# Kernel tuning notes

Hardware: AMD Instinct MI355X
Metric: run time of the kernel (lower is better)

## Reference

```python
import jax, jax.numpy as jnp
import numpy as np

DIM = 128
IND_DIM = 5
HEADS = 4
DIM_HEAD = 32
HIDDEN = HEADS * DIM_HEAD  # 128
SCALE = DIM_HEAD ** -0.5


def setup_inputs() -> dict:
    key = jax.random.key(0)
    ks = jax.random.split(key, 6)
    b, n = 1, 512
    x = jax.random.normal(ks[0], (b, DIM, n), dtype=jnp.float32)
    indicator = jax.random.normal(ks[1], (b, IND_DIM, n, n), dtype=jnp.float32)
    # conv1d kernels with kernel_size=1 are just (out, in) matrices
    w_qkv = jax.random.normal(ks[2], (HIDDEN * 3, DIM), dtype=jnp.float32) * (DIM ** -0.5)
    w_ind = jax.random.normal(ks[3], (HIDDEN * 2, IND_DIM), dtype=jnp.float32) * (IND_DIM ** -0.5)
    w_out = jax.random.normal(ks[4], (DIM, HIDDEN), dtype=jnp.float32) * (HIDDEN ** -0.5)
    b_out = jax.random.normal(ks[5], (DIM,), dtype=jnp.float32) * 0.01
    return {"x": x, "indicator": indicator, "w_qkv": w_qkv,
            "w_ind": w_ind, "w_out": w_out, "b_out": b_out}


def reference(x, indicator, w_qkv, w_ind, w_out, b_out):
    b, c, n = x.shape
    h, dh = HEADS, DIM_HEAD
    # pointwise conv = channel matmul
    qkv = jnp.einsum('oc,bcn->bon', w_qkv, x)  # (b, 3*hidden, n)
    q, k, v = jnp.split(qkv, 3, axis=1)
    q = q.reshape(b, h, dh, n)
    k = k.reshape(b, h, dh, n)
    v = v.reshape(b, h, dh, n)
    ind = jnp.einsum('oc,bcij->boij', w_ind, indicator)  # (b, 2*hidden, n, n)
    ind_q, ind_k = jnp.split(ind, 2, axis=1)
    ind_q = ind_q.reshape(b, h, dh, n, n)
    ind_k = ind_k.reshape(b, h, dh, n, n)
    qq = (q[..., :, None] + ind_q) * SCALE        # (b, h, dh, n, n)
    kk = k[..., None, :] + ind_k                   # (b, h, dh, n, n)
    sim = jnp.einsum('bhdij,bhdij->bhij', qq, kk)  # (b, h, n, n)
    attn = jax.nn.softmax(sim, axis=-1)
    out = jnp.einsum('bhij,bhdj->bhdi', attn, v)   # (b, h, dh, n)
    out = out.reshape(b, h * dh, n)
    return jnp.einsum('oc,bcn->bon', w_out, out) + b_out[None, :, None]
```

## Files before the change

kernel.cpp:

```cpp
#include <hip/hip_runtime.h>
#include <math.h>

#define N      512
#define DIMC   128
#define HEADS  4
#define DH     32
#define INDC   5
#define SCALE  0.1767766952966369f

#define QKV_ROWS 384
#define AQ_BASE  384
#define AK_BASE  404
#define TOT_ROWS 424
#define NROW_BLK (TOT_ROWS / 4)

#define ROWS_F   0
#define MHS_F    (TOT_ROWS * N)
#define WOUTT_F  (MHS_F + 64)

__global__ __launch_bounds__(256) void pre_kernel(const float* __restrict__ w_qkv,
                                                  const float* __restrict__ w_ind,
                                                  const float* __restrict__ x,
                                                  const float* __restrict__ w_out,
                                                  float* __restrict__ ws) {
    const int bx = blockIdx.x;
    const int t  = threadIdx.x;
    float* rows   = ws + ROWS_F;
    float* MhS    = ws + MHS_F;
    float* w_outT = ws + WOUTT_F;

    if (bx == NROW_BLK) {
        __shared__ float mraw[HEADS * INDC * INDC];
        if (t < HEADS * INDC * INDC) {
            const int h = t / 25, c = (t / 5) % 5, cc = t % 5;
            float acc = 0.f;
            for (int d = 0; d < DH; ++d)
                acc = fmaf(w_ind[(h * DH + d) * INDC + c],
                           w_ind[(DIMC + h * DH + d) * INDC + cc], acc);
            mraw[t] = acc;
        }
        __syncthreads();
        if (t < 64) {
            const int h = t >> 4, idx = t & 15;
            const int PC[10]  = {0, 0, 0, 0, 1, 1, 1, 2, 2, 3};
            const int PCC[10] = {1, 2, 3, 4, 2, 3, 4, 3, 4, 4};
            float s = 0.f;
            if (idx < 5) {
                s = mraw[h * 25 + idx * 5 + idx];
            } else if (idx < 15) {
                const int c = PC[idx - 5], cc = PCC[idx - 5];
                s = mraw[h * 25 + c * 5 + cc] + mraw[h * 25 + cc * 5 + c];
            }
            MhS[h * 16 + idx] = s;
        }
        for (int idx = t; idx < DIMC * DIMC; idx += 256) {
            const int o = idx >> 7, c = idx & 127;
            w_outT[c * DIMC + o] = w_out[idx];
        }
        return;
    }

    __shared__ float ws2[4 * DIMC];
    const int o0 = bx * 4;
    for (int idx = t; idx < 4 * DIMC; idx += 256) {
        const int r = idx & 3, m = idx >> 2;
        const int row = o0 + r;
        float val;
        if (row < QKV_ROWS) {
            val = w_qkv[row * DIMC + m];
        } else if (row < AK_BASE) {
            const int rr = row - AQ_BASE, h = rr / INDC, c = rr % INDC;
            float acc = 0.f;
            for (int d = 0; d < DH; ++d)
                acc = fmaf(w_qkv[(h * DH + d) * DIMC + m],
                           w_ind[(DIMC + h * DH + d) * INDC + c], acc);
            val = acc;
        } else {
            const int rr = row - AK_BASE, h = rr / INDC, c = rr % INDC;
            float acc = 0.f;
            for (int d = 0; d < DH; ++d)
                acc = fmaf(w_qkv[(DIMC + h * DH + d) * DIMC + m],
                           w_ind[(h * DH + d) * INDC + c], acc);
            val = acc;
        }
        ws2[m * 4 + r] = val;
    }
    __syncthreads();

    const float2* x2 = (const float2*)x;
    float2 acc[4] = {{0.f,0.f},{0.f,0.f},{0.f,0.f},{0.f,0.f}};
#pragma unroll 8
    for (int c = 0; c < DIMC; ++c) {
        const float2 xv = x2[c * 256 + t];
        const float4 wv = *(const float4*)(ws2 + c * 4);
        acc[0].x = fmaf(wv.x, xv.x, acc[0].x); acc[0].y = fmaf(wv.x, xv.y, acc[0].y);
        acc[1].x = fmaf(wv.y, xv.x, acc[1].x); acc[1].y = fmaf(wv.y, xv.y, acc[1].y);
        acc[2].x = fmaf(wv.z, xv.x, acc[2].x); acc[2].y = fmaf(wv.z, xv.y, acc[2].y);
        acc[3].x = fmaf(wv.w, xv.x, acc[3].x); acc[3].y = fmaf(wv.w, xv.y, acc[3].y);
    }
#pragma unroll
    for (int r = 0; r < 4; ++r)
        ((float2*)(rows + (o0 + r) * N))[t] = acc[r];
}

__global__ __launch_bounds__(256) void attn_kernel(const float* __restrict__ ws,
                                                   const float* __restrict__ ind,
                                                   const float* __restrict__ b_out,
                                                   float* __restrict__ out) {
    const int i    = blockIdx.x;
    const int t    = threadIdx.x;
    const int lane = t & 63;
    const int wave = t >> 6;

    const float* rows   = ws + ROWS_F;
    const float* MhS    = ws + MHS_F;
    const float* w_outT = ws + WOUTT_F;

    const float* q  = rows;
    const float* k  = rows + DIMC * N;
    const float* v  = rows + 2 * DIMC * N;
    const float* Aq = rows + 3 * DIMC * N;
    const float* Ak = Aq + HEADS * INDC * N;

    __shared__ float qs[DIMC];
    __shared__ float aqs[HEADS * INDC];
    __shared__ float msS[HEADS * 16];
    __shared__ float ps[HEADS][N];
    __shared__ float red[HEADS][DH][64];
    __shared__ float red4[2][HEADS][4];
    __shared__ float attv[DIMC];
    __shared__ float outred[4][DIMC];

    if (t < DIMC) qs[t] = q[t * N + i];
    else if (t >= 128 && t < 128 + HEADS * INDC) aqs[t - 128] = Aq[(t - 128) * N + i];
    else if (t >= 160 && t < 160 + HEADS * 16) msS[t - 160] = MhS[t - 160];
    __syncthreads();

    float2 ic[INDC];
#pragma unroll
    for (int c = 0; c < INDC; ++c)
        ic[c] = ((const float2*)(ind + (c * N + i) * N))[t];

    float2 prod[15];
#pragma unroll
    for (int c = 0; c < INDC; ++c)
        prod[c] = make_float2(ic[c].x * ic[c].x, ic[c].y * ic[c].y);
    {
        int p = 5;
#pragma unroll
        for (int c = 0; c < INDC; ++c)
#pragma unroll
            for (int cc = c + 1; cc < INDC; ++cc, ++p)
                prod[p] = make_float2(ic[c].x * ic[cc].x, ic[c].y * ic[cc].y);
    }

    const float2* k2  = (const float2*)k;
    const float2* Ak2 = (const float2*)Ak;
    float2 sim[HEADS];
#pragma unroll
    for (int h = 0; h < HEADS; ++h) {
        float2 qk = {0.f, 0.f};
#pragma unroll
        for (int d4 = 0; d4 < DH / 4; ++d4) {
            const float4 qv = *(const float4*)(qs + h * DH + 4 * d4);
            float2 kv;
            kv = k2[(h * DH + 4 * d4 + 0) * 256 + t];
            qk.x = fmaf(qv.x, kv.x, qk.x); qk.y = fmaf(qv.x, kv.y, qk.y);
            kv = k2[(h * DH + 4 * d4 + 1) * 256 + t];
            qk.x = fmaf(qv.y, kv.x, qk.x); qk.y = fmaf(qv.y, kv.y, qk.y);
            kv = k2[(h * DH + 4 * d4 + 2) * 256 + t];
            qk.x = fmaf(qv.z, kv.x, qk.x); qk.y = fmaf(qv.z, kv.y, qk.y);
            kv = k2[(h * DH + 4 * d4 + 3) * 256 + t];
            qk.x = fmaf(qv.w, kv.x, qk.x); qk.y = fmaf(qv.w, kv.y, qk.y);
        }
        float2 lin = {0.f, 0.f};
#pragma unroll
        for (int c = 0; c < INDC; ++c) {
            const float2 akv = Ak2[(h * INDC + c) * 256 + t];
            const float aqv = aqs[h * INDC + c];
            lin.x = fmaf(aqv + akv.x, ic[c].x, lin.x);
            lin.y = fmaf(aqv + akv.y, ic[c].y, lin.y);
        }
        float2 quad = {0.f, 0.f};
#pragma unroll
        for (int p = 0; p < 15; ++p) {
            const float sv = msS[h * 16 + p];
            quad.x = fmaf(sv, prod[p].x, quad.x);
            quad.y = fmaf(sv, prod[p].y, quad.y);
        }
        sim[h].x = SCALE * (qk.x + lin.x + quad.x);
        sim[h].y = SCALE * (qk.y + lin.y + quad.y);
    }

#pragma unroll
    for (int h = 0; h < HEADS; ++h) {
        float m = fmaxf(sim[h].x, sim[h].y);
#pragma unroll
        for (int off = 32; off; off >>= 1) m = fmaxf(m, __shfl_down(m, off, 64));
        if (lane == 0) red4[0][h][wave] = m;
    }
    __syncthreads();
    float2 e[HEADS];
#pragma unroll
    for (int h = 0; h < HEADS; ++h) {
        const float m = fmaxf(fmaxf(red4[0][h][0], red4[0][h][1]),
                              fmaxf(red4[0][h][2], red4[0][h][3]));
        e[h].x = __expf(sim[h].x - m);
        e[h].y = __expf(sim[h].y - m);
        float s = e[h].x + e[h].y;
#pragma unroll
        for (int off = 32; off; off >>= 1) s += __shfl_down(s, off, 64);
        if (lane == 0) red4[1][h][wave] = s;
    }
    __syncthreads();
#pragma unroll
    for (int h = 0; h < HEADS; ++h) {
        const float s = (red4[1][h][0] + red4[1][h][1]) + (red4[1][h][2] + red4[1][h][3]);
        const float rs = 1.f / s;
        ((float2*)&ps[h][0])[t] = make_float2(e[h].x * rs, e[h].y * rs);
    }
    __syncthreads();

    {
        const int h = wave;
        float acc[DH];
#pragma unroll
        for (int d = 0; d < DH; ++d) acc[d] = 0.f;
        const float2* ps2 = (const float2*)&ps[h][0];
        const float2* v2  = (const float2*)v;
        for (int s = 0; s < 4; ++s) {
            const float2 p = ps2[lane + 64 * s];
#pragma unroll
            for (int d = 0; d < DH; ++d) {
                const float2 vv = v2[(h * DH + d) * 256 + lane + 64 * s];
                acc[d] = fmaf(p.x, vv.x, fmaf(p.y, vv.y, acc[d]));
            }
        }
#pragma unroll
        for (int d = 0; d < DH; ++d) red[h][d][lane ^ d] = acc[d];
        const int d = lane & 31, half = lane >> 5;
        float s = 0.f;
#pragma unroll
        for (int kk = 0; kk < 32; ++kk) s += red[h][d][(half * 32 + kk) ^ d];
        s += __shfl_down(s, 32, 64);
        if (lane < 32) attv[h * DH + d] = s;
    }
    __syncthreads();

    {
        const int po = t & 63;
        const int quarter = t >> 6;
        const float2* wT2 = (const float2*)w_outT;
        float2 acc2 = {0.f, 0.f};
#pragma unroll 8
        for (int c = quarter * 32; c < quarter * 32 + 32; ++c) {
            const float av = attv[c];
            const float2 wv = wT2[c * 64 + po];
            acc2.x = fmaf(wv.x, av, acc2.x);
            acc2.y = fmaf(wv.y, av, acc2.y);
        }
        ((float2*)&outred[quarter][0])[po] = acc2;
    }
    __syncthreads();
    if (t < DIMC)
        out[t * N + i] = ((outred[0][t] + outred[1][t]) + (outred[2][t] + outred[3][t]))
                         + b_out[t];
}

extern "C" void kernel_launch(void* const* d_in, const int* in_sizes, int n_in,
                              void* d_out, int out_size, void* d_ws, size_t ws_size,
                              hipStream_t stream) {
    const float* x         = (const float*)d_in[0];
    const float* indicator = (const float*)d_in[1];
    const float* w_qkv     = (const float*)d_in[2];
    const float* w_ind     = (const float*)d_in[3];
    const float* w_out     = (const float*)d_in[4];
    const float* b_out     = (const float*)d_in[5];
    float* out = (float*)d_out;
    float* ws  = (float*)d_ws;

    pre_kernel<<<NROW_BLK + 1, 256, 0, stream>>>(w_qkv, w_ind, x, w_out, ws);
    attn_kernel<<<N, 256, 0, stream>>>(ws, indicator, b_out, out);
}
```

Baseline: 117.4 us.

## Process two query rows per attention block and split pre-kernel columns

Measured after the change: 115.0 us. -2.0%, faster.

```diff
diff --git a/kernel.cpp b/kernel.cpp
--- a/kernel.cpp
+++ b/kernel.cpp
@@ -30,6 +30,7 @@
     float* w_outT = ws + WOUTT_F;
 
     if (bx == NROW_BLK) {
+        if (blockIdx.y != 0) return;
         __shared__ float mraw[HEADS * INDC * INDC];
         if (t < HEADS * INDC * INDC) {
             const int h = t / 25, c = (t / 5) % 5, cc = t % 5;
@@ -87,27 +88,26 @@
     }
     __syncthreads();
 
-    const float2* x2 = (const float2*)x;
-    float2 acc[4] = {{0.f,0.f},{0.f,0.f},{0.f,0.f},{0.f,0.f}};
+    const int i = blockIdx.y * 256 + t;
+    float acc[4] = {0.f, 0.f, 0.f, 0.f};
 #pragma unroll 8
     for (int c = 0; c < DIMC; ++c) {
-        const float2 xv = x2[c * 256 + t];
+        const float xv = x[c * N + i];
         const float4 wv = *(const float4*)(ws2 + c * 4);
-        acc[0].x = fmaf(wv.x, xv.x, acc[0].x); acc[0].y = fmaf(wv.x, xv.y, acc[0].y);
-        acc[1].x = fmaf(wv.y, xv.x, acc[1].x); acc[1].y = fmaf(wv.y, xv.y, acc[1].y);
-        acc[2].x = fmaf(wv.z, xv.x, acc[2].x); acc[2].y = fmaf(wv.z, xv.y, acc[2].y);
-        acc[3].x = fmaf(wv.w, xv.x, acc[3].x); acc[3].y = fmaf(wv.w, xv.y, acc[3].y);
-    }
-#pragma unroll
-    for (int r = 0; r < 4; ++r)
-        ((float2*)(rows + (o0 + r) * N))[t] = acc[r];
+        acc[0] = fmaf(wv.x, xv, acc[0]);
+        acc[1] = fmaf(wv.y, xv, acc[1]);
+        acc[2] = fmaf(wv.z, xv, acc[2]);
+        acc[3] = fmaf(wv.w, xv, acc[3]);
+    }
+#pragma unroll
+    for (int r = 0; r < 4; ++r) rows[(o0 + r) * N + i] = acc[r];
 }
 
 __global__ __launch_bounds__(256) void attn_kernel(const float* __restrict__ ws,
                                                    const float* __restrict__ ind,
                                                    const float* __restrict__ b_out,
                                                    float* __restrict__ out) {
-    const int i    = blockIdx.x;
+    const int i0   = blockIdx.x * 2;
     const int t    = threadIdx.x;
     const int lane = t & 63;
     const int wave = t >> 6;
@@ -122,128 +122,159 @@
     const float* Aq = rows + 3 * DIMC * N;
     const float* Ak = Aq + HEADS * INDC * N;
 
-    __shared__ float qs[DIMC];
-    __shared__ float aqs[HEADS * INDC];
+    __shared__ float qs[2][DIMC];
+    __shared__ float aqs[2][HEADS * INDC];
     __shared__ float msS[HEADS * 16];
-    __shared__ float ps[HEADS][N];
+    __shared__ float ps[HEADS][2][N];
     __shared__ float red[HEADS][DH][64];
-    __shared__ float red4[2][HEADS][4];
-    __shared__ float attv[DIMC];
-    __shared__ float outred[4][DIMC];
-
-    if (t < DIMC) qs[t] = q[t * N + i];
-    else if (t >= 128 && t < 128 + HEADS * INDC) aqs[t - 128] = Aq[(t - 128) * N + i];
-    else if (t >= 160 && t < 160 + HEADS * 16) msS[t - 160] = MhS[t - 160];
-    __syncthreads();
-
-    float2 ic[INDC];
-#pragma unroll
-    for (int c = 0; c < INDC; ++c)
-        ic[c] = ((const float2*)(ind + (c * N + i) * N))[t];
-
-    float2 prod[15];
-#pragma unroll
-    for (int c = 0; c < INDC; ++c)
-        prod[c] = make_float2(ic[c].x * ic[c].x, ic[c].y * ic[c].y);
+    __shared__ float red4[2][HEADS][2][4];
+    __shared__ float attv[2][DIMC];
+    __shared__ float outred[4][2][DIMC];
+
+    if (t < DIMC) qs[0][t] = q[t * N + i0];
+    else          qs[1][t - DIMC] = q[(t - DIMC) * N + i0 + 1];
+    if (t < 2 * HEADS * INDC) {
+        const int ii = t / (HEADS * INDC), r = t % (HEADS * INDC);
+        aqs[ii][r] = Aq[r * N + i0 + ii];
+    } else if (t < 2 * HEADS * INDC + 64) {
+        msS[t - 2 * HEADS * INDC] = MhS[t - 2 * HEADS * INDC];
+    }
+    __syncthreads();
+
+    float2 ic0[INDC], ic1[INDC];
+#pragma unroll
+    for (int c = 0; c < INDC; ++c) {
+        ic0[c] = ((const float2*)(ind + (c * N + i0) * N))[t];
+        ic1[c] = ((const float2*)(ind + (c * N + i0 + 1) * N))[t];
+    }
+    float2 prod0[15], prod1[15];
+#pragma unroll
+    for (int c = 0; c < INDC; ++c) {
+        prod0[c] = make_float2(ic0[c].x * ic0[c].x, ic0[c].y * ic0[c].y);
+        prod1[c] = make_float2(ic1[c].x * ic1[c].x, ic1[c].y * ic1[c].y);
+    }
     {
         int p = 5;
 #pragma unroll
         for (int c = 0; c < INDC; ++c)
 #pragma unroll
-            for (int cc = c + 1; cc < INDC; ++cc, ++p)
-                prod[p] = make_float2(ic[c].x * ic[cc].x, ic[c].y * ic[cc].y);
+            for (int cc = c + 1; cc < INDC; ++cc, ++p) {
+                prod0[p] = make_float2(ic0[c].x * ic0[cc].x, ic0[c].y * ic0[cc].y);
+                prod1[p] = make_float2(ic1[c].x * ic1[cc].x, ic1[c].y * ic1[cc].y);
+            }
     }
 
     const float2* k2  = (const float2*)k;
     const float2* Ak2 = (const float2*)Ak;
-    float2 sim[HEADS];
+    float2 sim0[HEADS], sim1[HEADS];
 #pragma unroll
     for (int h = 0; h < HEADS; ++h) {
-        float2 qk = {0.f, 0.f};
-#pragma unroll
-        for (int d4 = 0; d4 < DH / 4; ++d4) {
-            const float4 qv = *(const float4*)(qs + h * DH + 4 * d4);
-            float2 kv;
-            kv = k2[(h * DH + 4 * d4 + 0) * 256 + t];
-            qk.x = fmaf(qv.x, kv.x, qk.x); qk.y = fmaf(qv.x, kv.y, qk.y);
-            kv = k2[(h * DH + 4 * d4 + 1) * 256 + t];
-            qk.x = fmaf(qv.y, kv.x, qk.x); qk.y = fmaf(qv.y, kv.y, qk.y);
-            kv = k2[(h * DH + 4 * d4 + 2) * 256 + t];
-            qk.x = fmaf(qv.z, kv.x, qk.x); qk.y = fmaf(qv.z, kv.y, qk.y);
-            kv = k2[(h * DH + 4 * d4 + 3) * 256 + t];
-            qk.x = fmaf(qv.w, kv.x, qk.x); qk.y = fmaf(qv.w, kv.y, qk.y);
-        }
-        float2 lin = {0.f, 0.f};
+        float2 qk0 = {0.f, 0.f}, qk1 = {0.f, 0.f};
+#pragma unroll
+        for (int d = 0; d < DH; ++d) {
+            const float2 kv = k2[(h * DH + d) * 256 + t];
+            const float q0 = qs[0][h * DH + d], q1 = qs[1][h * DH + d];
+            qk0.x = fmaf(q0, kv.x, qk0.x); qk0.y = fmaf(q0, kv.y, qk0.y);
+            qk1.x = fmaf(q1, kv.x, qk1.x); qk1.y = fmaf(q1, kv.y, qk1.y);
+        }
+        float2 lin0 = {0.f, 0.f}, lin1 = {0.f, 0.f};
 #pragma unroll
         for (int c = 0; c < INDC; ++c) {
             const float2 akv = Ak2[(h * INDC + c) * 256 + t];
-            const float aqv = aqs[h * INDC + c];
-            lin.x = fmaf(aqv + akv.x, ic[c].x, lin.x);
-            lin.y = fmaf(aqv + akv.y, ic[c].y, lin.y);
-        }
-        float2 quad = {0.f, 0.f};
+            const float a0 = aqs[0][h * INDC + c], a1 = aqs[1][h * INDC + c];
+            lin0.x = fmaf(a0 + akv.x, ic0[c].x, lin0.x);
+            lin0.y = fmaf(a0 + akv.y, ic0[c].y, lin0.y);
+            lin1.x = fmaf(a1 + akv.x, ic1[c].x, lin1.x);
+            lin1.y = fmaf(a1 + akv.y, ic1[c].y, lin1.y);
+        }
+        float2 qd0 = {0.f, 0.f}, qd1 = {0.f, 0.f};
 #pragma unroll
         for (int p = 0; p < 15; ++p) {
             const float sv = msS[h * 16 + p];
-            quad.x = fmaf(sv, prod[p].x, quad.x);
-            quad.y = fmaf(sv, prod[p].y, quad.y);
-        }
-        sim[h].x = SCALE * (qk.x + lin.x + quad.x);
-        sim[h].y = SCALE * (qk.y + lin.y + quad.y);
+            qd0.x = fmaf(sv, prod0[p].x, qd0.x); qd0.y = fmaf(sv, prod0[p].y, qd0.y);
+            qd1.x = fmaf(sv, prod1[p].x, qd1.x); qd1.y = fmaf(sv, prod1[p].y, qd1.y);
+        }
+        sim0[h].x = SCALE * (qk0.x + lin0.x + qd0.x);
+        sim0[h].y = SCALE * (qk0.y + lin0.y + qd0.y);
+        sim1[h].x = SCALE * (qk1.x + lin1.x + qd1.x);
+        sim1[h].y = SCALE * (qk1.y + lin1.y + qd1.y);
     }
 
 #pragma unroll
     for (int h = 0; h < HEADS; ++h) {
-        float m = fmaxf(sim[h].x, sim[h].y);
-#pragma unroll
-        for (int off = 32; off; off >>= 1) m = fmaxf(m, __shfl_down(m, off, 64));
-        if (lane == 0) red4[0][h][wave] = m;
-    }
-    __syncthreads();
-    float2 e[HEADS];
+        float m0 = fmaxf(sim0[h].x, sim0[h].y);
+        float m1 = fmaxf(sim1[h].x, sim1[h].y);
+#pragma unroll
+        for (int off = 32; off; off >>= 1) {
+            m0 = fmaxf(m0, __shfl_down(m0, off, 64));
+            m1 = fmaxf(m1, __shfl_down(m1, off, 64));
+        }
+        if (lane == 0) { red4[0][h][0][wave] = m0; red4[0][h][1][wave] = m1; }
+    }
+    __syncthreads();
+    float2 e0[HEADS], e1[HEADS];
 #pragma unroll
     for (int h = 0; h < HEADS; ++h) {
-        const float m = fmaxf(fmaxf(red4[0][h][0], red4[0][h][1]),
-                              fmaxf(red4[0][h][2], red4[0][h][3]));
-        e[h].x = __expf(sim[h].x - m);
-        e[h].y = __expf(sim[h].y - m);
-        float s = e[h].x + e[h].y;
-#pragma unroll
-        for (int off = 32; off; off >>= 1) s += __shfl_down(s, off, 64);
-        if (lane == 0) red4[1][h][wave] = s;
+        const float m0 = fmaxf(fmaxf(red4[0][h][0][0], red4[0][h][0][1]),
+                               fmaxf(red4[0][h][0][2], red4[0][h][0][3]));
+        const float m1 = fmaxf(fmaxf(red4[0][h][1][0], red4[0][h][1][1]),
+                               fmaxf(red4[0][h][1][2], red4[0][h][1][3]));
+        e0[h].x = __expf(sim0[h].x - m0); e0[h].y = __expf(sim0[h].y - m0);
+        e1[h].x = __expf(sim1[h].x - m1); e1[h].y = __expf(sim1[h].y - m1);
+        float s0 = e0[h].x + e0[h].y, s1 = e1[h].x + e1[h].y;
+#pragma unroll
+        for (int off = 32; off; off >>= 1) {
+            s0 += __shfl_down(s0, off, 64);
+            s1 += __shfl_down(s1, off, 64);
+        }
+        if (lane == 0) { red4[1][h][0][wave] = s0; red4[1][h][1][wave] = s1; }
     }
     __syncthreads();
 #pragma unroll
     for (int h = 0; h < HEADS; ++h) {
-        const float s = (red4[1][h][0] + red4[1][h][1]) + (red4[1][h][2] + red4[1][h][3]);
-        const float rs = 1.f / s;
-        ((float2*)&ps[h][0])[t] = make_float2(e[h].x * rs, e[h].y * rs);
+        const float s0 = (red4[1][h][0][0] + red4[1][h][0][1]) +
+                         (red4[1][h][0][2] + red4[1][h][0][3]);
+        const float s1 = (red4[1][h][1][0] + red4[1][h][1][1]) +
+                         (red4[1][h][1][2] + red4[1][h][1][3]);
+        const float r0 = 1.f / s0, r1 = 1.f / s1;
+        ((float2*)&ps[h][0][0])[t] = make_float2(e0[h].x * r0, e0[h].y * r0);
+        ((float2*)&ps[h][1][0])[t] = make_float2(e1[h].x * r1, e1[h].y * r1);
     }
     __syncthreads();
 
     {
         const int h = wave;
-        float acc[DH];
-#pragma unroll
-        for (int d = 0; d < DH; ++d) acc[d] = 0.f;
-        const float2* ps2 = (const float2*)&ps[h][0];
+        float acc0[DH], acc1[DH];
+#pragma unroll
+        for (int d = 0; d < DH; ++d) { acc0[d] = 0.f; acc1[d] = 0.f; }
+        const float2* ps0 = (const float2*)&ps[h][0][0];
+        const float2* ps1 = (const float2*)&ps[h][1][0];
         const float2* v2  = (const float2*)v;
         for (int s = 0; s < 4; ++s) {
-            const float2 p = ps2[lane + 64 * s];
+            const float2 p0 = ps0[lane + 64 * s];
+            const float2 p1 = ps1[lane + 64 * s];
 #pragma unroll
             for (int d = 0; d < DH; ++d) {
                 const float2 vv = v2[(h * DH + d) * 256 + lane + 64 * s];
-                acc[d] = fmaf(p.x, vv.x, fmaf(p.y, vv.y, acc[d]));
+                acc0[d] = fmaf(p0.x, vv.x, fmaf(p0.y, vv.y, acc0[d]));
+                acc1[d] = fmaf(p1.x, vv.x, fmaf(p1.y, vv.y, acc1[d]));
             }
         }
-#pragma unroll
-        for (int d = 0; d < DH; ++d) red[h][d][lane ^ d] = acc[d];
         const int d = lane & 31, half = lane >> 5;
+#pragma unroll
+        for (int dd = 0; dd < DH; ++dd) red[h][dd][lane ^ dd] = acc0[dd];
         float s = 0.f;
 #pragma unroll
         for (int kk = 0; kk < 32; ++kk) s += red[h][d][(half * 32 + kk) ^ d];
         s += __shfl_down(s, 32, 64);
-        if (lane < 32) attv[h * DH + d] = s;
+        if (lane < 32) attv[0][h * DH + d] = s;
+#pragma unroll
+        for (int dd = 0; dd < DH; ++dd) red[h][dd][lane ^ dd] = acc1[dd];
+        s = 0.f;
+#pragma unroll
+        for (int kk = 0; kk < 32; ++kk) s += red[h][d][(half * 32 + kk) ^ d];
+        s += __shfl_down(s, 32, 64);
+        if (lane < 32) attv[1][h * DH + d] = s;
     }
     __syncthreads();
 
@@ -251,20 +282,23 @@
         const int po = t & 63;
         const int quarter = t >> 6;
         const float2* wT2 = (const float2*)w_outT;
-        float2 acc2 = {0.f, 0.f};
+        float2 a0 = {0.f, 0.f}, a1 = {0.f, 0.f};
 #pragma unroll 8
         for (int c = quarter * 32; c < quarter * 32 + 32; ++c) {
-            const float av = attv[c];
             const float2 wv = wT2[c * 64 + po];
-            acc2.x = fmaf(wv.x, av, acc2.x);
-            acc2.y = fmaf(wv.y, av, acc2.y);
-        }
-        ((float2*)&outred[quarter][0])[po] = acc2;
-    }
-    __syncthreads();
-    if (t < DIMC)
-        out[t * N + i] = ((outred[0][t] + outred[1][t]) + (outred[2][t] + outred[3][t]))
-                         + b_out[t];
+            const float av0 = attv[0][c], av1 = attv[1][c];
+            a0.x = fmaf(wv.x, av0, a0.x); a0.y = fmaf(wv.y, av0, a0.y);
+            a1.x = fmaf(wv.x, av1, a1.x); a1.y = fmaf(wv.y, av1, a1.y);
+        }
+        ((float2*)&outred[quarter][0][0])[po] = a0;
+        ((float2*)&outred[quarter][1][0])[po] = a1;
+    }
+    __syncthreads();
+    {
+        const int o = t & 127, ii = t >> 7;
+        out[o * N + i0 + ii] = ((outred[0][ii][o] + outred[1][ii][o]) +
+                                (outred[2][ii][o] + outred[3][ii][o])) + b_out[o];
+    }
 }
 
 extern "C" void kernel_launch(void* const* d_in, const int* in_sizes, int n_in,
@@ -279,6 +313,6 @@
     float* out = (float*)d_out;
     float* ws  = (float*)d_ws;
 
-    pre_kernel<<<NROW_BLK + 1, 256, 0, stream>>>(w_qkv, w_ind, x, w_out, ws);
-    attn_kernel<<<N, 256, 0, stream>>>(ws, indicator, b_out, out);
+    pre_kernel<<<dim3(NROW_BLK + 1, 2), 256, 0, stream>>>(w_qkv, w_ind, x, w_out, ws);
+    attn_kernel<<<N / 2, 256, 0, stream>>>(ws, indicator, b_out, out);
 }
```
